# Optimization experiments

Hardware: AMD Instinct MI355X
Metric: run time of the kernel (lower is better)

The kernel has to match this reference:

```python
import jax, jax.numpy as jnp
import numpy as np

ALPHA_MAX = 0.1


def setup_inputs() -> dict:
    key = jax.random.key(0)
    ks = jax.random.split(key, 9)
    B, M, L = 256, 3, 100000
    A, H = 4096, 512
    return {
        "x": jax.random.uniform(ks[0], (B, M, L), dtype=jnp.float32),  # log1p scores, non-negative
        "active_idx": jax.random.randint(ks[1], (A,), 0, L, dtype=jnp.int64 if jax.config.jax_enable_x64 else jnp.int32),
        "global_logits": jnp.log(jnp.full((M,), 1.0 / M, dtype=jnp.float32) + 1e-12),
        "delta_w": 0.01 * jax.random.normal(ks[2], (M, L), dtype=jnp.float32),
        "bias": 0.01 * jax.random.normal(ks[3], (L,), dtype=jnp.float32),
        "log_alpha": jnp.float32(-3.0),
        "hidden_w": jax.random.normal(ks[4], (H, M * A), dtype=jnp.float32) * (1.0 / np.sqrt(M * A)),
        "hidden_b": 0.01 * jax.random.normal(ks[5], (H,), dtype=jnp.float32),
        "delta_layer_w": jax.random.normal(ks[6], (A, H), dtype=jnp.float32) * (1.0 / np.sqrt(H)),
        "delta_layer_b": 0.01 * jax.random.normal(ks[7], (A,), dtype=jnp.float32),
    }


def reference(x, active_idx, global_logits, delta_w, bias, log_alpha,
              hidden_w, hidden_b, delta_layer_w, delta_layer_b):
    B = x.shape[0]
    # base logits: elementwise weighted sum over the 3 models, per-label weights
    w_eff = jax.nn.softmax(global_logits)[:, None] + delta_w          # (M, L)
    logits = jnp.einsum("bml,ml->bl", x, w_eff) + bias                # (B, L)
    # gather active labels -> 2-layer MLP (dropout is identity in eval)
    x_active = x[:, :, active_idx].reshape(B, -1)                     # (B, M*A)
    h = jax.nn.relu(x_active @ hidden_w.T + hidden_b)                 # (B, H)
    delta_active = h @ delta_layer_w.T + delta_layer_b                # (B, A)
    # scaled scatter-add back into full logits (duplicates accumulate)
    alpha = ALPHA_MAX * jax.nn.sigmoid(log_alpha)
    logits = logits.at[:, active_idx].add(alpha * delta_active)
    return logits
```

## Files before the change

### kernel.cpp

```cpp
#include <hip/hip_runtime.h>
#include <math.h>

#define B_ 256
#define M_ 3
#define L_ 100000
#define A_ 4096
#define H_ 512
#define MA_ (M_*A_)
#define K1_ MA_
#define NZ_ 16
#define KC1_ (K1_/NZ_)
#define BCHUNK_ 4

typedef __attribute__((ext_vector_type(8))) short bf16x8;
typedef __attribute__((ext_vector_type(8))) unsigned short u16x8;
typedef __attribute__((ext_vector_type(4))) float f32x4;

static __device__ __forceinline__ float4 ld4(const float* p) {
    return *reinterpret_cast<const float4*>(p);
}
static __device__ __forceinline__ void st4(float* p, float4 v) {
    *reinterpret_cast<float4*>(p) = v;
}
static __device__ __forceinline__ unsigned short f2bf(float f) {
    unsigned u = __float_as_uint(f);
    unsigned r = (u + 0x7FFFu + ((u >> 16) & 1u)) >> 16;
    return (unsigned short)r;
}
static __device__ __forceinline__ bf16x8 cvt8(float4 a, float4 b) {
    bf16x8 o;
    o[0] = (short)f2bf(a.x); o[1] = (short)f2bf(a.y);
    o[2] = (short)f2bf(a.z); o[3] = (short)f2bf(a.w);
    o[4] = (short)f2bf(b.x); o[5] = (short)f2bf(b.y);
    o[6] = (short)f2bf(b.z); o[7] = (short)f2bf(b.w);
    return o;
}
static __device__ __forceinline__ float getc(const float4& v, int c) {
    switch (c) { case 0: return v.x; case 1: return v.y; case 2: return v.z; default: return v.w; }
}

__global__ void init_head(int* __restrict__ head) {
    int i = blockIdx.x * blockDim.x + threadIdx.x;
    if (i < L_ / 4) *reinterpret_cast<int4*>(head + i * 4) = make_int4(-1, -1, -1, -1);
}

__global__ void build_chain(const int* __restrict__ idx, int* __restrict__ head,
                            int* __restrict__ next) {
    int a = blockIdx.x * blockDim.x + threadIdx.x;
    if (a < A_) next[a] = atomicExch(&head[idx[a]], a);
}

__global__ void f32_to_bf16(const float* __restrict__ in, unsigned short* __restrict__ out, int n8) {
    int i = blockIdx.x * blockDim.x + threadIdx.x;
    if (i >= n8) return;
    float4 v0 = ld4(in + (size_t)i * 8);
    float4 v1 = ld4(in + (size_t)i * 8 + 4);
    u16x8 o;
    o[0] = f2bf(v0.x); o[1] = f2bf(v0.y); o[2] = f2bf(v0.z); o[3] = f2bf(v0.w);
    o[4] = f2bf(v1.x); o[5] = f2bf(v1.y); o[6] = f2bf(v1.z); o[7] = f2bf(v1.w);
    *reinterpret_cast<u16x8*>(out + (size_t)i * 8) = o;
}

__global__ __launch_bounds__(256) void logits_gather(
    const float* __restrict__ x, const float* __restrict__ gl,
    const float* __restrict__ dw, const float* __restrict__ bias,
    const int* __restrict__ head, const int* __restrict__ next,
    float* __restrict__ logits, unsigned short* __restrict__ xa) {
    const int L4 = L_ / 4;
    int i = blockIdx.x * blockDim.x + threadIdx.x;
    if (i >= L4) return;
    int l = i * 4;
    int b0 = blockIdx.y * BCHUNK_;

    float g0 = gl[0], g1 = gl[1], g2 = gl[2];
    float mx = fmaxf(g0, fmaxf(g1, g2));
    float e0 = expf(g0 - mx), e1 = expf(g1 - mx), e2 = expf(g2 - mx);
    float inv = 1.0f / (e0 + e1 + e2);
    float s0 = e0 * inv, s1 = e1 * inv, s2 = e2 * inv;

    float4 d0 = ld4(dw + l);
    float4 d1 = ld4(dw + L_ + l);
    float4 d2 = ld4(dw + 2 * L_ + l);
    float4 bb = ld4(bias + l);
    float4 w0 = make_float4(s0 + d0.x, s0 + d0.y, s0 + d0.z, s0 + d0.w);
    float4 w1 = make_float4(s1 + d1.x, s1 + d1.y, s1 + d1.z, s1 + d1.w);
    float4 w2 = make_float4(s2 + d2.x, s2 + d2.y, s2 + d2.z, s2 + d2.w);

    int4 heads = *reinterpret_cast<const int4*>(head + l);

    float4 X[BCHUNK_][3];
    #pragma unroll
    for (int c = 0; c < BCHUNK_; ++c) {
        const float* xb = x + (size_t)(b0 + c) * M_ * L_ + l;
        X[c][0] = ld4(xb);
        X[c][1] = ld4(xb + L_);
        X[c][2] = ld4(xb + 2 * L_);
    }
    #pragma unroll
    for (int c = 0; c < BCHUNK_; ++c) {
        float4 o;
        o.x = X[c][0].x * w0.x + X[c][1].x * w1.x + X[c][2].x * w2.x + bb.x;
        o.y = X[c][0].y * w0.y + X[c][1].y * w1.y + X[c][2].y * w2.y + bb.y;
        o.z = X[c][0].z * w0.z + X[c][1].z * w1.z + X[c][2].z * w2.z + bb.z;
        o.w = X[c][0].w * w0.w + X[c][1].w * w1.w + X[c][2].w * w2.w + bb.w;
        st4(logits + (size_t)(b0 + c) * L_ + l, o);
    }

    int hs[4] = {heads.x, heads.y, heads.z, heads.w};
    #pragma unroll
    for (int c = 0; c < 4; ++c) {
        int a = hs[c];
        while (a >= 0) {
            #pragma unroll
            for (int b = 0; b < BCHUNK_; ++b) {
                unsigned short* xab = xa + (size_t)(b0 + b) * MA_;
                xab[a]          = f2bf(getc(X[b][0], c));
                xab[A_ + a]     = f2bf(getc(X[b][1], c));
                xab[2 * A_ + a] = f2bf(getc(X[b][2], c));
            }
            a = next[a];
        }
    }
}

__global__ __launch_bounds__(256) void gemm1_mfma(
    const unsigned short* __restrict__ Xa, const unsigned short* __restrict__ W,
    float* __restrict__ part) {
    int tid = threadIdx.x;
    int wave = tid >> 6, lane = tid & 63;
    int row0 = blockIdx.x * 64 + (wave >> 1) * 32;
    int col0 = blockIdx.y * 64 + (wave & 1) * 32;
    int k0 = blockIdx.z * KC1_;
    int lr = lane & 15;
    int lk = (lane >> 4) * 8;
    const unsigned short* pa0 = Xa + (size_t)(row0 + lr) * K1_ + k0 + lk;
    const unsigned short* pa1 = pa0 + (size_t)16 * K1_;
    const unsigned short* pb0 = W + (size_t)(col0 + lr) * K1_ + k0 + lk;
    const unsigned short* pb1 = pb0 + (size_t)16 * K1_;
    f32x4 acc00 = {0.f,0.f,0.f,0.f}, acc01 = {0.f,0.f,0.f,0.f};
    f32x4 acc10 = {0.f,0.f,0.f,0.f}, acc11 = {0.f,0.f,0.f,0.f};
    #pragma unroll 4
    for (int k = 0; k < KC1_; k += 32) {
        bf16x8 a0 = *reinterpret_cast<const bf16x8*>(pa0 + k);
        bf16x8 a1 = *reinterpret_cast<const bf16x8*>(pa1 + k);
        bf16x8 b0 = *reinterpret_cast<const bf16x8*>(pb0 + k);
        bf16x8 b1 = *reinterpret_cast<const bf16x8*>(pb1 + k);
        acc00 = __builtin_amdgcn_mfma_f32_16x16x32_bf16(a0, b0, acc00, 0, 0, 0);
        acc01 = __builtin_amdgcn_mfma_f32_16x16x32_bf16(a0, b1, acc01, 0, 0, 0);
        acc10 = __builtin_amdgcn_mfma_f32_16x16x32_bf16(a1, b0, acc10, 0, 0, 0);
        acc11 = __builtin_amdgcn_mfma_f32_16x16x32_bf16(a1, b1, acc11, 0, 0, 0);
    }
    float* base = part + (size_t)blockIdx.z * B_ * H_;
    #pragma unroll
    for (int j = 0; j < 4; ++j) {
        int r = (lane >> 4) * 4 + j;
        base[(size_t)(row0 + r) * H_ + col0 + lr]           = acc00[j];
        base[(size_t)(row0 + r) * H_ + col0 + 16 + lr]      = acc01[j];
        base[(size_t)(row0 + 16 + r) * H_ + col0 + lr]      = acc10[j];
        base[(size_t)(row0 + 16 + r) * H_ + col0 + 16 + lr] = acc11[j];
    }
}

__global__ void reduce_relu(const float* __restrict__ part,
                            const float* __restrict__ hb,
                            unsigned short* __restrict__ h) {
    int t = blockIdx.x * blockDim.x + threadIdx.x;
    if (t >= B_ * H_) return;
    int n = t & (H_ - 1);
    float s = hb[n];
    #pragma unroll
    for (int z = 0; z < NZ_; ++z) s += part[(size_t)z * B_ * H_ + t];
    h[t] = f2bf(fmaxf(s, 0.0f));
}

__global__ __launch_bounds__(256) void gemm2_scatter(
    const unsigned short* __restrict__ Hm, const float* __restrict__ W2,
    const float* __restrict__ b2, const float* __restrict__ la,
    const int* __restrict__ idx, float* __restrict__ logits) {
    int tid = threadIdx.x;
    int wave = tid >> 6, lane = tid & 63;
    int row0 = blockIdx.x * 64 + (wave >> 1) * 32;
    int col0 = blockIdx.y * 64 + (wave & 1) * 32;
    int lr = lane & 15;
    int lk = (lane >> 4) * 8;
    const unsigned short* pa0 = Hm + (size_t)(row0 + lr) * H_ + lk;
    const unsigned short* pa1 = pa0 + (size_t)16 * H_;
    const float* pb0 = W2 + (size_t)(col0 + lr) * H_ + lk;
    const float* pb1 = pb0 + (size_t)16 * H_;
    f32x4 acc00 = {0.f,0.f,0.f,0.f}, acc01 = {0.f,0.f,0.f,0.f};
    f32x4 acc10 = {0.f,0.f,0.f,0.f}, acc11 = {0.f,0.f,0.f,0.f};
    #pragma unroll 4
    for (int k = 0; k < H_; k += 32) {
        bf16x8 a0 = *reinterpret_cast<const bf16x8*>(pa0 + k);
        bf16x8 a1 = *reinterpret_cast<const bf16x8*>(pa1 + k);
        bf16x8 b0 = cvt8(ld4(pb0 + k), ld4(pb0 + k + 4));
        bf16x8 b1 = cvt8(ld4(pb1 + k), ld4(pb1 + k + 4));
        acc00 = __builtin_amdgcn_mfma_f32_16x16x32_bf16(a0, b0, acc00, 0, 0, 0);
        acc01 = __builtin_amdgcn_mfma_f32_16x16x32_bf16(a0, b1, acc01, 0, 0, 0);
        acc10 = __builtin_amdgcn_mfma_f32_16x16x32_bf16(a1, b0, acc10, 0, 0, 0);
        acc11 = __builtin_amdgcn_mfma_f32_16x16x32_bf16(a1, b1, acc11, 0, 0, 0);
    }
    float alpha = 0.1f / (1.0f + expf(-la[0]));
    int c0 = col0 + lr, c1 = col0 + 16 + lr;
    int l0 = idx[c0], l1 = idx[c1];
    float bias0 = b2[c0], bias1 = b2[c1];
    #pragma unroll
    for (int j = 0; j < 4; ++j) {
        int r = (lane >> 4) * 4 + j;
        atomicAdd(&logits[(size_t)(row0 + r) * L_ + l0],      alpha * (acc00[j] + bias0));
        atomicAdd(&logits[(size_t)(row0 + r) * L_ + l1],      alpha * (acc01[j] + bias1));
        atomicAdd(&logits[(size_t)(row0 + 16 + r) * L_ + l0], alpha * (acc10[j] + bias0));
        atomicAdd(&logits[(size_t)(row0 + 16 + r) * L_ + l1], alpha * (acc11[j] + bias1));
    }
}

static inline size_t align256(size_t x) { return (x + 255) & ~(size_t)255; }

extern "C" void kernel_launch(void* const* d_in, const int* in_sizes, int n_in,
                              void* d_out, int out_size, void* d_ws, size_t ws_size,
                              hipStream_t stream) {
    const float* x    = (const float*)d_in[0];
    const int*   idx  = (const int*)d_in[1];
    const float* gl   = (const float*)d_in[2];
    const float* dw   = (const float*)d_in[3];
    const float* bias = (const float*)d_in[4];
    const float* la   = (const float*)d_in[5];
    const float* hw   = (const float*)d_in[6];
    const float* hb   = (const float*)d_in[7];
    const float* w2   = (const float*)d_in[8];
    const float* b2   = (const float*)d_in[9];
    float* logits = (float*)d_out;

    char* ws = (char*)d_ws;
    int* head = (int*)ws;                      ws += align256((size_t)L_ * 4);
    int* next = (int*)ws;                      ws += align256((size_t)A_ * 4);
    unsigned short* xa = (unsigned short*)ws;  ws += align256((size_t)B_ * MA_ * 2);
    unsigned short* hwb = (unsigned short*)ws; ws += align256((size_t)H_ * MA_ * 2);
    float* part = (float*)ws;                  ws += align256((size_t)NZ_ * B_ * H_ * 4);
    unsigned short* h = (unsigned short*)ws;   ws += align256((size_t)B_ * H_ * 2);

    init_head<<<(L_ / 4 + 255) / 256, 256, 0, stream>>>(head);
    build_chain<<<(A_ + 255) / 256, 256, 0, stream>>>(idx, head, next);

    f32_to_bf16<<<(H_ * MA_ / 8 + 255) / 256, 256, 0, stream>>>(hw, hwb, H_ * MA_ / 8);

    dim3 g1((L_ / 4 + 255) / 256, B_ / BCHUNK_);
    logits_gather<<<g1, 256, 0, stream>>>(x, gl, dw, bias, head, next, logits, xa);

    gemm1_mfma<<<dim3(B_ / 64, H_ / 64, NZ_), 256, 0, stream>>>(xa, hwb, part);
    reduce_relu<<<(B_ * H_ + 255) / 256, 256, 0, stream>>>(part, hb, h);
    gemm2_scatter<<<dim3(B_ / 64, A_ / 64), 256, 0, stream>>>(h, w2, b2, la, idx, logits);
}
```

Baseline: 210.6 us.

## Fuse weight conversions into logits kernel, replace duplicate chains with fixup pass

Merges the hidden_w and delta_layer_w bf16 conversions into one launch alongside the logits/gather work, so those independent streams run concurrently. The linked-list duplicate handling is replaced by a single head entry per label plus a separate fixup kernel that copies gathered values for duplicate indices. Streaming x loads and logits stores now use nontemporal hints, and gemm2 reads pre-converted bf16 weights instead of converting per tile. This adds one extra launch and a second pass over xa for duplicates, and build_head relies on an unordered race that picks any one writer.

```diff
diff --git a/kernel.cpp b/kernel.cpp
--- a/kernel.cpp
+++ b/kernel.cpp
@@ -12,65 +12,74 @@
 #define KC1_ (K1_/NZ_)
 #define BCHUNK_ 4
 
+#define NB_LG_   6272
+#define NB_LGX_  98
+#define NB_HW_   3072
+#define NB_W2_   1024
+
 typedef __attribute__((ext_vector_type(8))) short bf16x8;
 typedef __attribute__((ext_vector_type(8))) unsigned short u16x8;
 typedef __attribute__((ext_vector_type(4))) float f32x4;
-
-static __device__ __forceinline__ float4 ld4(const float* p) {
-    return *reinterpret_cast<const float4*>(p);
-}
-static __device__ __forceinline__ void st4(float* p, float4 v) {
-    *reinterpret_cast<float4*>(p) = v;
+typedef __attribute__((ext_vector_type(4))) int i32x4;
+
+static __device__ __forceinline__ f32x4 ld4(const float* p) {
+    return *reinterpret_cast<const f32x4*>(p);
+}
+static __device__ __forceinline__ f32x4 ld4nt(const float* p) {
+    return __builtin_nontemporal_load(reinterpret_cast<const f32x4*>(p));
+}
+static __device__ __forceinline__ void st4nt(float* p, f32x4 v) {
+    __builtin_nontemporal_store(v, reinterpret_cast<f32x4*>(p));
 }
 static __device__ __forceinline__ unsigned short f2bf(float f) {
     unsigned u = __float_as_uint(f);
     unsigned r = (u + 0x7FFFu + ((u >> 16) & 1u)) >> 16;
     return (unsigned short)r;
 }
-static __device__ __forceinline__ bf16x8 cvt8(float4 a, float4 b) {
-    bf16x8 o;
-    o[0] = (short)f2bf(a.x); o[1] = (short)f2bf(a.y);
-    o[2] = (short)f2bf(a.z); o[3] = (short)f2bf(a.w);
-    o[4] = (short)f2bf(b.x); o[5] = (short)f2bf(b.y);
-    o[6] = (short)f2bf(b.z); o[7] = (short)f2bf(b.w);
-    return o;
-}
-static __device__ __forceinline__ float getc(const float4& v, int c) {
-    switch (c) { case 0: return v.x; case 1: return v.y; case 2: return v.z; default: return v.w; }
-}
 
 __global__ void init_head(int* __restrict__ head) {
     int i = blockIdx.x * blockDim.x + threadIdx.x;
-    if (i < L_ / 4) *reinterpret_cast<int4*>(head + i * 4) = make_int4(-1, -1, -1, -1);
-}
-
-__global__ void build_chain(const int* __restrict__ idx, int* __restrict__ head,
-                            int* __restrict__ next) {
+    if (i < L_ / 4) {
+        i32x4 m1 = {-1, -1, -1, -1};
+        *reinterpret_cast<i32x4*>(head + i * 4) = m1;
+    }
+}
+
+__global__ void build_head(const int* __restrict__ idx, int* __restrict__ head) {
     int a = blockIdx.x * blockDim.x + threadIdx.x;
-    if (a < A_) next[a] = atomicExch(&head[idx[a]], a);
-}
-
-__global__ void f32_to_bf16(const float* __restrict__ in, unsigned short* __restrict__ out, int n8) {
-    int i = blockIdx.x * blockDim.x + threadIdx.x;
-    if (i >= n8) return;
-    float4 v0 = ld4(in + (size_t)i * 8);
-    float4 v1 = ld4(in + (size_t)i * 8 + 4);
-    u16x8 o;
-    o[0] = f2bf(v0.x); o[1] = f2bf(v0.y); o[2] = f2bf(v0.z); o[3] = f2bf(v0.w);
-    o[4] = f2bf(v1.x); o[5] = f2bf(v1.y); o[6] = f2bf(v1.z); o[7] = f2bf(v1.w);
-    *reinterpret_cast<u16x8*>(out + (size_t)i * 8) = o;
-}
-
-__global__ __launch_bounds__(256) void logits_gather(
+    if (a < A_) head[idx[a]] = a;
+}
+
+__global__ __launch_bounds__(256) void mega(
     const float* __restrict__ x, const float* __restrict__ gl,
     const float* __restrict__ dw, const float* __restrict__ bias,
-    const int* __restrict__ head, const int* __restrict__ next,
-    float* __restrict__ logits, unsigned short* __restrict__ xa) {
+    const int* __restrict__ head,
+    float* __restrict__ logits, unsigned short* __restrict__ xa,
+    const float* __restrict__ hw, unsigned short* __restrict__ hwb,
+    const float* __restrict__ w2, unsigned short* __restrict__ w2b) {
+    int bid = blockIdx.x;
+    int tid = threadIdx.x;
+
+    if (bid >= NB_LG_) {
+        const float* src;
+        unsigned short* dst;
+        int i;
+        if (bid < NB_LG_ + NB_HW_) { src = hw; dst = hwb; i = (bid - NB_LG_) * 256 + tid; }
+        else                       { src = w2; dst = w2b; i = (bid - NB_LG_ - NB_HW_) * 256 + tid; }
+        f32x4 v0 = ld4nt(src + (size_t)i * 8);
+        f32x4 v1 = ld4nt(src + (size_t)i * 8 + 4);
+        u16x8 o;
+        o[0] = f2bf(v0.x); o[1] = f2bf(v0.y); o[2] = f2bf(v0.z); o[3] = f2bf(v0.w);
+        o[4] = f2bf(v1.x); o[5] = f2bf(v1.y); o[6] = f2bf(v1.z); o[7] = f2bf(v1.w);
+        *reinterpret_cast<u16x8*>(dst + (size_t)i * 8) = o;
+        return;
+    }
+
     const int L4 = L_ / 4;
-    int i = blockIdx.x * blockDim.x + threadIdx.x;
+    int i = (bid % NB_LGX_) * 256 + tid;
     if (i >= L4) return;
     int l = i * 4;
-    int b0 = blockIdx.y * BCHUNK_;
+    int b0 = (bid / NB_LGX_) * BCHUNK_;
 
     float g0 = gl[0], g1 = gl[1], g2 = gl[2];
     float mx = fmaxf(g0, fmaxf(g1, g2));
@@ -78,49 +87,57 @@
     float inv = 1.0f / (e0 + e1 + e2);
     float s0 = e0 * inv, s1 = e1 * inv, s2 = e2 * inv;
 
-    float4 d0 = ld4(dw + l);
-    float4 d1 = ld4(dw + L_ + l);
-    float4 d2 = ld4(dw + 2 * L_ + l);
-    float4 bb = ld4(bias + l);
-    float4 w0 = make_float4(s0 + d0.x, s0 + d0.y, s0 + d0.z, s0 + d0.w);
-    float4 w1 = make_float4(s1 + d1.x, s1 + d1.y, s1 + d1.z, s1 + d1.w);
-    float4 w2 = make_float4(s2 + d2.x, s2 + d2.y, s2 + d2.z, s2 + d2.w);
-
-    int4 heads = *reinterpret_cast<const int4*>(head + l);
-
-    float4 X[BCHUNK_][3];
+    f32x4 d0 = ld4(dw + l);
+    f32x4 d1 = ld4(dw + L_ + l);
+    f32x4 d2 = ld4(dw + 2 * L_ + l);
+    f32x4 bb = ld4(bias + l);
+    f32x4 w0 = d0 + s0;
+    f32x4 w1 = d1 + s1;
+    f32x4 w2v = d2 + s2;
+
+    i32x4 heads = *reinterpret_cast<const i32x4*>(head + l);
+
+    f32x4 X[BCHUNK_][3];
     #pragma unroll
     for (int c = 0; c < BCHUNK_; ++c) {
         const float* xb = x + (size_t)(b0 + c) * M_ * L_ + l;
-        X[c][0] = ld4(xb);
-        X[c][1] = ld4(xb + L_);
-        X[c][2] = ld4(xb + 2 * L_);
+        X[c][0] = ld4nt(xb);
+        X[c][1] = ld4nt(xb + L_);
+        X[c][2] = ld4nt(xb + 2 * L_);
     }
     #pragma unroll
     for (int c = 0; c < BCHUNK_; ++c) {
-        float4 o;
-        o.x = X[c][0].x * w0.x + X[c][1].x * w1.x + X[c][2].x * w2.x + bb.x;
-        o.y = X[c][0].y * w0.y + X[c][1].y * w1.y + X[c][2].y * w2.y + bb.y;
-        o.z = X[c][0].z * w0.z + X[c][1].z * w1.z + X[c][2].z * w2.z + bb.z;
-        o.w = X[c][0].w * w0.w + X[c][1].w * w1.w + X[c][2].w * w2.w + bb.w;
-        st4(logits + (size_t)(b0 + c) * L_ + l, o);
-    }
-
-    int hs[4] = {heads.x, heads.y, heads.z, heads.w};
+        f32x4 o = X[c][0] * w0 + X[c][1] * w1 + X[c][2] * w2v + bb;
+        st4nt(logits + (size_t)(b0 + c) * L_ + l, o);
+    }
+
     #pragma unroll
     for (int c = 0; c < 4; ++c) {
-        int a = hs[c];
-        while (a >= 0) {
+        int a = heads[c];
+        if (a >= 0) {
             #pragma unroll
             for (int b = 0; b < BCHUNK_; ++b) {
                 unsigned short* xab = xa + (size_t)(b0 + b) * MA_;
-                xab[a]          = f2bf(getc(X[b][0], c));
-                xab[A_ + a]     = f2bf(getc(X[b][1], c));
-                xab[2 * A_ + a] = f2bf(getc(X[b][2], c));
+                xab[a]          = f2bf(X[b][0][c]);
+                xab[A_ + a]     = f2bf(X[b][1][c]);
+                xab[2 * A_ + a] = f2bf(X[b][2][c]);
             }
-            a = next[a];
         }
     }
+}
+
+__global__ void fixup(const int* __restrict__ idx, const int* __restrict__ head,
+                      unsigned short* __restrict__ xa) {
+    int t = blockIdx.x * blockDim.x + threadIdx.x;
+    if (t >= B_ * A_) return;
+    int a = t & (A_ - 1);
+    int b = t >> 12;
+    int ha = head[idx[a]];
+    if (ha == a) return;
+    unsigned short* xab = xa + (size_t)b * MA_;
+    xab[a]          = xab[ha];
+    xab[A_ + a]     = xab[A_ + ha];
+    xab[2 * A_ + a] = xab[2 * A_ + ha];
 }
 
 __global__ __launch_bounds__(256) void gemm1_mfma(
@@ -174,7 +191,7 @@
 }
 
 __global__ __launch_bounds__(256) void gemm2_scatter(
-    const unsigned short* __restrict__ Hm, const float* __restrict__ W2,
+    const unsigned short* __restrict__ Hm, const unsigned short* __restrict__ W2,
     const float* __restrict__ b2, const float* __restrict__ la,
     const int* __restrict__ idx, float* __restrict__ logits) {
     int tid = threadIdx.x;
@@ -185,16 +202,16 @@
     int lk = (lane >> 4) * 8;
     const unsigned short* pa0 = Hm + (size_t)(row0 + lr) * H_ + lk;
     const unsigned short* pa1 = pa0 + (size_t)16 * H_;
-    const float* pb0 = W2 + (size_t)(col0 + lr) * H_ + lk;
-    const float* pb1 = pb0 + (size_t)16 * H_;
+    const unsigned short* pb0 = W2 + (size_t)(col0 + lr) * H_ + lk;
+    const unsigned short* pb1 = pb0 + (size_t)16 * H_;
     f32x4 acc00 = {0.f,0.f,0.f,0.f}, acc01 = {0.f,0.f,0.f,0.f};
     f32x4 acc10 = {0.f,0.f,0.f,0.f}, acc11 = {0.f,0.f,0.f,0.f};
     #pragma unroll 4
     for (int k = 0; k < H_; k += 32) {
         bf16x8 a0 = *reinterpret_cast<const bf16x8*>(pa0 + k);
         bf16x8 a1 = *reinterpret_cast<const bf16x8*>(pa1 + k);
-        bf16x8 b0 = cvt8(ld4(pb0 + k), ld4(pb0 + k + 4));
-        bf16x8 b1 = cvt8(ld4(pb1 + k), ld4(pb1 + k + 4));
+        bf16x8 b0 = *reinterpret_cast<const bf16x8*>(pb0 + k);
+        bf16x8 b1 = *reinterpret_cast<const bf16x8*>(pb1 + k);
         acc00 = __builtin_amdgcn_mfma_f32_16x16x32_bf16(a0, b0, acc00, 0, 0, 0);
         acc01 = __builtin_amdgcn_mfma_f32_16x16x32_bf16(a0, b1, acc01, 0, 0, 0);
         acc10 = __builtin_amdgcn_mfma_f32_16x16x32_bf16(a1, b0, acc10, 0, 0, 0);
@@ -233,21 +250,21 @@
 
     char* ws = (char*)d_ws;
     int* head = (int*)ws;                      ws += align256((size_t)L_ * 4);
-    int* next = (int*)ws;                      ws += align256((size_t)A_ * 4);
     unsigned short* xa = (unsigned short*)ws;  ws += align256((size_t)B_ * MA_ * 2);
     unsigned short* hwb = (unsigned short*)ws; ws += align256((size_t)H_ * MA_ * 2);
+    unsigned short* w2b = (unsigned short*)ws; ws += align256((size_t)A_ * H_ * 2);
     float* part = (float*)ws;                  ws += align256((size_t)NZ_ * B_ * H_ * 4);
     unsigned short* h = (unsigned short*)ws;   ws += align256((size_t)B_ * H_ * 2);
 
     init_head<<<(L_ / 4 + 255) / 256, 256, 0, stream>>>(head);
-    build_chain<<<(A_ + 255) / 256, 256, 0, stream>>>(idx, head, next);
-
-    f32_to_bf16<<<(H_ * MA_ / 8 + 255) / 256, 256, 0, stream>>>(hw, hwb, H_ * MA_ / 8);
-
-    dim3 g1((L_ / 4 + 255) / 256, B_ / BCHUNK_);
-    logits_gather<<<g1, 256, 0, stream>>>(x, gl, dw, bias, head, next, logits, xa);
+    build_head<<<(A_ + 255) / 256, 256, 0, stream>>>(idx, head);
+
+    mega<<<NB_LG_ + NB_HW_ + NB_W2_, 256, 0, stream>>>(
+        x, gl, dw, bias, head, logits, xa, hw, hwb, w2, w2b);
+
+    fixup<<<(B_ * A_ + 255) / 256, 256, 0, stream>>>(idx, head, xa);
 
     gemm1_mfma<<<dim3(B_ / 64, H_ / 64, NZ_), 256, 0, stream>>>(xa, hwb, part);
     reduce_relu<<<(B_ * H_ + 255) / 256, 256, 0, stream>>>(part, hb, h);
-    gemm2_scatter<<<dim3(B_ / 64, A_ / 64), 256, 0, stream>>>(h, w2, b2, la, idx, logits);
-}
+    gemm2_scatter<<<dim3(B_ / 64, A_ / 64), 256, 0, stream>>>(h, w2b, b2, la, idx, logits);
+}
```

Result: faster. 202.3 us (-4.0%).
